# Kernel optimization log

Measured on AMD Instinct MI355X. Metric: run time of the kernel, lower is better.

Reference implementation:

```python
import jax, jax.numpy as jnp
import numpy as np
from jax import lax


def setup_inputs() -> dict:
    key = jax.random.key(0)
    ks = jax.random.split(key, 6)
    B, S, E, T = 64, 512, 1024, 9
    pretraining_embed = jax.random.normal(ks[0], (B, S, E), dtype=jnp.float32)
    tags = jax.random.randint(ks[1], (B, S), 0, T, dtype=jnp.int64)
    mask = jnp.ones((B, S), dtype=jnp.int32)  # torchcrf requires mask[:, 0] == 1
    W = jax.random.normal(ks[2], (T, E), dtype=jnp.float32) * 0.02
    b = jnp.zeros((T,), dtype=jnp.float32)
    start_transitions = jax.random.normal(ks[3], (T,), dtype=jnp.float32) * 0.1
    end_transitions = jax.random.normal(ks[4], (T,), dtype=jnp.float32) * 0.1
    transitions = jax.random.normal(ks[5], (T, T), dtype=jnp.float32) * 0.1
    return dict(pretraining_embed=pretraining_embed, tags=tags, mask=mask, W=W, b=b,
                start_transitions=start_transitions, end_transitions=end_transitions,
                transitions=transitions)


def _crf_llh(emission, tags, mask, start_transitions, end_transitions, transitions):
    # emission: [B,S,T] log-probs; tags: [B,S] int; mask: [B,S] int (mask[:,0]=1)
    maskf = mask.astype(emission.dtype)
    # --- numerator: score of the gold path ---
    em_tag = jnp.take_along_axis(emission, tags[:, :, None], axis=2)[..., 0]  # [B,S]
    trans_tag = transitions[tags[:, :-1], tags[:, 1:]]                        # [B,S-1]
    numerator = (start_transitions[tags[:, 0]] + em_tag[:, 0]
                 + jnp.sum(maskf[:, 1:] * (trans_tag + em_tag[:, 1:]), axis=1))
    seq_last = jnp.sum(mask, axis=1) - 1                                      # [B]
    last_tags = jnp.take_along_axis(tags, seq_last[:, None], axis=1)[:, 0]
    numerator = numerator + end_transitions[last_tags]
    # --- denominator: forward algorithm (logsumexp DP over time) ---
    def step(score, xs):
        em_t, m_t = xs  # [B,T], [B]
        # [B, prev T, next T] -> logsumexp over prev
        nxt = jax.nn.logsumexp(score[:, :, None] + transitions[None, :, :] + em_t[:, None, :], axis=1)
        score = jnp.where(m_t[:, None] > 0, nxt, score)
        return score, None
    init = start_transitions[None, :] + emission[:, 0]  # [B,T]
    score, _ = lax.scan(step, init,
                        (jnp.swapaxes(emission[:, 1:], 0, 1), jnp.swapaxes(mask[:, 1:], 0, 1)))
    denominator = jax.nn.logsumexp(score + end_transitions[None, :], axis=1)  # [B]
    # torchcrf default reduction='sum'; .mean() of the resulting scalar is a no-op
    return jnp.sum(numerator - denominator)


def reference(pretraining_embed, tags, mask, W, b, start_transitions, end_transitions, transitions):
    tag_space = jnp.einsum('bse,te->bst', pretraining_embed, W) + b  # hidden2tag
    emission = jax.nn.log_softmax(tag_space, axis=2)
    log_likelihood = _crf_llh(emission, tags, mask, start_transitions, end_transitions, transitions)
    return (log_likelihood, emission)
```

## Files before the change

kernel.cpp:

```cpp
#include <hip/hip_runtime.h>


#define BB 64
#define SS 512
#define EE 1024
#define TT 9

__global__ __launch_bounds__(256) void emis_kernel(
    const float* __restrict__ embed,
    const float* __restrict__ W,
    const float* __restrict__ bias,
    float* __restrict__ out)
{
    if (blockIdx.x == 0 && threadIdx.x == 0) out[0] = 0.0f;

    const int wid  = threadIdx.x >> 6;
    const int lane = threadIdx.x & 63;
    const int row0 = blockIdx.x * 16 + wid * 4;

    float acc[4][TT];
#pragma unroll
    for (int r = 0; r < 4; ++r)
#pragma unroll
        for (int t = 0; t < TT; ++t) acc[r][t] = 0.0f;

#pragma unroll
    for (int k = 0; k < 4; ++k) {
        const int off = k * 256 + 4 * lane;
        float4 w[TT];
#pragma unroll
        for (int t = 0; t < TT; ++t)
            w[t] = *(const float4*)(W + t * EE + off);
#pragma unroll
        for (int r = 0; r < 4; ++r) {
            const float4 x = *(const float4*)(embed + (size_t)(row0 + r) * EE + off);
#pragma unroll
            for (int t = 0; t < TT; ++t)
                acc[r][t] += x.x * w[t].x + x.y * w[t].y + x.z * w[t].z + x.w * w[t].w;
        }
    }

#pragma unroll
    for (int r = 0; r < 4; ++r) {
#pragma unroll
        for (int t = 0; t < TT; ++t) {
#pragma unroll
            for (int o = 32; o > 0; o >>= 1)
                acc[r][t] += __shfl_xor(acc[r][t], o, 64);
            acc[r][t] += bias[t];
        }
        float m = acc[r][0];
#pragma unroll
        for (int t = 1; t < TT; ++t) m = fmaxf(m, acc[r][t]);
        float ssum = 0.0f;
#pragma unroll
        for (int t = 0; t < TT; ++t) ssum += __expf(acc[r][t] - m);
        const float lse = m + __logf(ssum);

        float val = acc[r][0];
#pragma unroll
        for (int t = 1; t < TT; ++t) val = (lane == t) ? acc[r][t] : val;
        if (lane < TT)
            out[1 + (size_t)(row0 + r) * TT + lane] = val - lse;
    }
}

__global__ __launch_bounds__(256) void crf_chunk(
    const float* __restrict__ outbase,
    const int* __restrict__ mask,
    const float* __restrict__ trans,
    float* __restrict__ ws)
{
    const int gw   = (blockIdx.x * 256 + threadIdx.x) >> 6;
    const int lane = threadIdx.x & 63;
    const int b = gw >> 6;
    const int c = gw & 63;
    const int i = (lane < TT) ? lane : 0;

    const float* em = outbase + 1 + (size_t)b * SS * TT;

    float E[TT * TT];
#pragma unroll
    for (int e = 0; e < TT * TT; ++e) E[e] = __expf(trans[e]);

    const int s0 = 8 * c + 1;
    float R[TT];
    {
        float p[TT];
#pragma unroll
        for (int j = 0; j < TT; ++j) p[j] = __expf(em[s0 * TT + j]);
        const int mk = mask[b * SS + s0];
#pragma unroll
        for (int k = 0; k < TT; ++k)
            R[k] = mk ? (E[i * TT + k] * p[k]) : ((k == i) ? 1.0f : 0.0f);
    }
#pragma unroll
    for (int d = 1; d < 8; ++d) {
        const int s = s0 + d;
        const bool valid = (s < SS);
        const int sc = valid ? s : (SS - 1);
        float p[TT];
#pragma unroll
        for (int j = 0; j < TT; ++j) p[j] = __expf(em[sc * TT + j]);
        const int mk = valid ? mask[b * SS + sc] : 0;

        float nR[TT];
#pragma unroll
        for (int j = 0; j < TT; ++j) {
            float a = 0.0f;
#pragma unroll
            for (int k = 0; k < TT; ++k) a += R[k] * E[k * TT + j];
            nR[j] = a * p[j];
        }
#pragma unroll
        for (int j = 0; j < TT; ++j) R[j] = mk ? nR[j] : R[j];
    }
    if (lane < TT) {
#pragma unroll
        for (int j = 0; j < TT; ++j)
            ws[(size_t)gw * 81 + i * TT + j] = R[j];
    }
}

__global__ __launch_bounds__(256) void crf_final(
    const float* __restrict__ outbase,
    const int* __restrict__ tags,
    const int* __restrict__ mask,
    const float* __restrict__ start_t,
    const float* __restrict__ end_t,
    const float* __restrict__ trans,
    const float* __restrict__ ws,
    float* __restrict__ out)
{
    __shared__ float mats[127 * 81];
    __shared__ float red[4];
    __shared__ float redm[4];

    const int b = blockIdx.x;
    const int tid = threadIdx.x;
    const int lane = tid & 63, wid = tid >> 6;
    const float* em = outbase + 1 + (size_t)b * SS * TT;

    for (int idx = tid; idx < 64 * 81; idx += 256)
        mats[idx] = ws[(size_t)b * 64 * 81 + idx];

    float num = 0.0f;
    int msum = 0;
    for (int s = tid; s < SS; s += 256) {
        const int mk = mask[b * SS + s];
        msum += mk;
        const int tg = tags[b * SS + s];
        if (s == 0) {
            num += start_t[tg] + em[tg];
        } else {
            const int tp = tags[b * SS + s - 1];
            num += (float)mk * (trans[tp * TT + tg] + em[s * TT + tg]);
        }
    }
#pragma unroll
    for (int o = 32; o > 0; o >>= 1) {
        num += __shfl_xor(num, o, 64);
        msum += __shfl_xor(msum, o, 64);
    }
    if (lane == 0) { red[wid] = num; redm[wid] = (float)msum; }
    __syncthreads();

    int inOff = 0, outOff = 64;
    for (int n = 32; n >= 1; n >>= 1) {
        for (int c = wid; c < n; c += 4) {
            const float* A  = mats + (inOff + 2 * c) * 81;
            const float* Bm = mats + (inOff + 2 * c + 1) * 81;
            float* C = mats + (outOff + c) * 81;
            int e = lane;
            int ii = e / 9, jj = e - ii * 9;
            float a = 0.0f;
#pragma unroll
            for (int k = 0; k < TT; ++k) a += A[ii * 9 + k] * Bm[k * 9 + jj];
            C[e] = a;
            if (lane < 17) {
                e = 64 + lane; ii = e / 9; jj = e - ii * 9;
                float a2 = 0.0f;
#pragma unroll
                for (int k = 0; k < TT; ++k) a2 += A[ii * 9 + k] * Bm[k * 9 + jj];
                C[e] = a2;
            }
        }
        __syncthreads();
        inOff = outOff; outOff += n;
    }

    if (wid == 0) {
        const float* Mt = mats + 126 * 81;
        float v0[TT];
#pragma unroll
        for (int i2 = 0; i2 < TT; ++i2) v0[i2] = __expf(start_t[i2] + em[i2]);
        const int j = (lane < TT) ? lane : 0;
        float cs = 0.0f;
#pragma unroll
        for (int i2 = 0; i2 < TT; ++i2) cs += v0[i2] * Mt[i2 * 9 + j];
        float val = cs * __expf(end_t[j]);
        if (lane >= TT) val = 0.0f;
#pragma unroll
        for (int o = 8; o > 0; o >>= 1) val += __shfl_xor(val, o, 64);
        if (lane == 0) {
            const float den = __logf(val);
            float numT = red[0] + red[1] + red[2] + red[3];
            const int ms = (int)(redm[0] + redm[1] + redm[2] + redm[3]);
            numT += end_t[tags[b * SS + (ms - 1)]];
            atomicAdd(out, numT - den);
        }
    }
}

extern "C" void kernel_launch(void* const* d_in, const int* in_sizes, int n_in,
                              void* d_out, int out_size, void* d_ws, size_t ws_size,
                              hipStream_t stream) {
    const float* embed   = (const float*)d_in[0];
    const int*   tags    = (const int*)d_in[1];
    const int*   mask    = (const int*)d_in[2];
    const float* W       = (const float*)d_in[3];
    const float* bias    = (const float*)d_in[4];
    const float* start_t = (const float*)d_in[5];
    const float* end_t   = (const float*)d_in[6];
    const float* trans   = (const float*)d_in[7];
    float* out = (float*)d_out;
    float* ws  = (float*)d_ws;

    emis_kernel<<<2048, 256, 0, stream>>>(embed, W, bias, out);
    crf_chunk<<<1024, 256, 0, stream>>>(out, mask, trans, ws);
    crf_final<<<BB, 256, 0, stream>>>(out, tags, mask, start_t, end_t, trans, ws, out);
}
```

Measured before the change: 250.2 us.

## Fuse CRF chunk transfer-matrix computation into final reduction kernel

Merges the per-chunk transfer-matrix kernel into the final per-batch kernel, so each of the 64 blocks (now 512 threads) computes its 64 chunk matrices directly into shared memory. Seven chunks are packed per wavefront (9 lanes each) instead of one chunk per 64-lane wave. This removes a kernel launch and the workspace round trip through global memory. The trade-off is only 64 blocks doing the chunk work, which lowers parallelism for that phase, and the numerator loop now assumes exactly 512 threads cover S.

```diff
diff --git a/kernel.cpp b/kernel.cpp
--- a/kernel.cpp
+++ b/kernel.cpp
@@ -65,96 +65,83 @@
     }
 }
 
-__global__ __launch_bounds__(256) void crf_chunk(
-    const float* __restrict__ outbase,
-    const int* __restrict__ mask,
-    const float* __restrict__ trans,
-    float* __restrict__ ws)
-{
-    const int gw   = (blockIdx.x * 256 + threadIdx.x) >> 6;
-    const int lane = threadIdx.x & 63;
-    const int b = gw >> 6;
-    const int c = gw & 63;
-    const int i = (lane < TT) ? lane : 0;
-
-    const float* em = outbase + 1 + (size_t)b * SS * TT;
-
-    float E[TT * TT];
-#pragma unroll
-    for (int e = 0; e < TT * TT; ++e) E[e] = __expf(trans[e]);
-
-    const int s0 = 8 * c + 1;
-    float R[TT];
-    {
-        float p[TT];
-#pragma unroll
-        for (int j = 0; j < TT; ++j) p[j] = __expf(em[s0 * TT + j]);
-        const int mk = mask[b * SS + s0];
-#pragma unroll
-        for (int k = 0; k < TT; ++k)
-            R[k] = mk ? (E[i * TT + k] * p[k]) : ((k == i) ? 1.0f : 0.0f);
-    }
-#pragma unroll
-    for (int d = 1; d < 8; ++d) {
-        const int s = s0 + d;
-        const bool valid = (s < SS);
-        const int sc = valid ? s : (SS - 1);
-        float p[TT];
-#pragma unroll
-        for (int j = 0; j < TT; ++j) p[j] = __expf(em[sc * TT + j]);
-        const int mk = valid ? mask[b * SS + sc] : 0;
-
-        float nR[TT];
-#pragma unroll
-        for (int j = 0; j < TT; ++j) {
-            float a = 0.0f;
-#pragma unroll
-            for (int k = 0; k < TT; ++k) a += R[k] * E[k * TT + j];
-            nR[j] = a * p[j];
-        }
-#pragma unroll
-        for (int j = 0; j < TT; ++j) R[j] = mk ? nR[j] : R[j];
-    }
-    if (lane < TT) {
-#pragma unroll
-        for (int j = 0; j < TT; ++j)
-            ws[(size_t)gw * 81 + i * TT + j] = R[j];
-    }
-}
-
-__global__ __launch_bounds__(256) void crf_final(
+__global__ __launch_bounds__(512) void crf_fused(
     const float* __restrict__ outbase,
     const int* __restrict__ tags,
     const int* __restrict__ mask,
     const float* __restrict__ start_t,
     const float* __restrict__ end_t,
     const float* __restrict__ trans,
-    const float* __restrict__ ws,
     float* __restrict__ out)
 {
     __shared__ float mats[127 * 81];
-    __shared__ float red[4];
-    __shared__ float redm[4];
-
-    const int b = blockIdx.x;
-    const int tid = threadIdx.x;
-    const int lane = tid & 63, wid = tid >> 6;
+    __shared__ float red[8];
+    __shared__ float redm[8];
+
+    const int b    = blockIdx.x;
+    const int tid  = threadIdx.x;
+    const int lane = tid & 63;
+    const int wid  = tid >> 6;
     const float* em = outbase + 1 + (size_t)b * SS * TT;
 
-    for (int idx = tid; idx < 64 * 81; idx += 256)
-        mats[idx] = ws[(size_t)b * 64 * 81 + idx];
+    float E[TT * TT];
+#pragma unroll
+    for (int e = 0; e < TT * TT; ++e) E[e] = __expf(trans[e]);
+
+    const int g = lane / TT;
+    const int i = lane - g * TT;
+    const bool lact = (lane < 63);
+
+    for (int grp = wid; grp < 10; grp += 8) {
+        const int c = grp * 7 + g;
+        const bool cact = lact && (c < 64);
+        const int cc = cact ? c : 0;
+        const int s0 = 8 * cc + 1;
+
+        float R[TT];
+#pragma unroll
+        for (int k = 0; k < TT; ++k) R[k] = (k == i) ? 1.0f : 0.0f;
+
+#pragma unroll
+        for (int d = 0; d < 8; ++d) {
+            const int s = s0 + d;
+            const bool valid = (s < SS);
+            const int sc = valid ? s : (SS - 1);
+            float p[TT];
+#pragma unroll
+            for (int j = 0; j < TT; ++j) p[j] = __expf(em[sc * TT + j]);
+            const int mk = (cact && valid) ? mask[b * SS + sc] : 0;
+
+            float nR[TT];
+#pragma unroll
+            for (int j = 0; j < TT; ++j) {
+                float a = 0.0f;
+#pragma unroll
+                for (int k = 0; k < TT; ++k) a += R[k] * E[k * TT + j];
+                nR[j] = a * p[j];
+            }
+#pragma unroll
+            for (int j = 0; j < TT; ++j) R[j] = mk ? nR[j] : R[j];
+        }
+        if (cact) {
+#pragma unroll
+            for (int j = 0; j < TT; ++j)
+                mats[c * 81 + i * TT + j] = R[j];
+        }
+    }
 
     float num = 0.0f;
     int msum = 0;
-    for (int s = tid; s < SS; s += 256) {
+    {
+        const int s = tid;
         const int mk = mask[b * SS + s];
-        msum += mk;
+        msum = mk;
         const int tg = tags[b * SS + s];
         if (s == 0) {
-            num += start_t[tg] + em[tg];
+            num = start_t[tg] + em[tg];
         } else {
             const int tp = tags[b * SS + s - 1];
-            num += (float)mk * (trans[tp * TT + tg] + em[s * TT + tg]);
+            num = (float)mk * (trans[tp * TT + tg] + em[s * TT + tg]);
         }
     }
 #pragma unroll
@@ -167,7 +154,7 @@
 
     int inOff = 0, outOff = 64;
     for (int n = 32; n >= 1; n >>= 1) {
-        for (int c = wid; c < n; c += 4) {
+        for (int c = wid; c < n; c += 8) {
             const float* A  = mats + (inOff + 2 * c) * 81;
             const float* Bm = mats + (inOff + 2 * c + 1) * 81;
             float* C = mats + (outOff + c) * 81;
@@ -204,8 +191,10 @@
         for (int o = 8; o > 0; o >>= 1) val += __shfl_xor(val, o, 64);
         if (lane == 0) {
             const float den = __logf(val);
-            float numT = red[0] + red[1] + red[2] + red[3];
-            const int ms = (int)(redm[0] + redm[1] + redm[2] + redm[3]);
+            float numT = red[0] + red[1] + red[2] + red[3]
+                       + red[4] + red[5] + red[6] + red[7];
+            const int ms = (int)(redm[0] + redm[1] + redm[2] + redm[3]
+                               + redm[4] + redm[5] + redm[6] + redm[7]);
             numT += end_t[tags[b * SS + (ms - 1)]];
             atomicAdd(out, numT - den);
         }
@@ -224,9 +213,8 @@
     const float* end_t   = (const float*)d_in[6];
     const float* trans   = (const float*)d_in[7];
     float* out = (float*)d_out;
-    float* ws  = (float*)d_ws;
+    (void)d_ws; (void)ws_size;
 
     emis_kernel<<<2048, 256, 0, stream>>>(embed, W, bias, out);
-    crf_chunk<<<1024, 256, 0, stream>>>(out, mask, trans, ws);
-    crf_final<<<BB, 256, 0, stream>>>(out, tags, mask, start_t, end_t, trans, ws, out);
+    crf_fused<<<BB, 512, 0, stream>>>(out, tags, mask, start_t, end_t, trans, out);
 }
```

After: 223.5 us. -10.7%, faster.
